# Kernel tuning notes

Hardware: AMD Instinct MI355X
Metric: run time of the kernel (lower is better)

The kernel has to match this reference:

```python
import jax, jax.numpy as jnp
import numpy as np

B_, T_, DIM = 32, 65536, 64
L_ = T_ // DIM                       # 1024 tokens after unfold
EXPAND, HEADDIM, DSTATE, DCONV = 4, 64, 16, 4
DIN = EXPAND * DIM                   # 256
NHEADS = DIN // HEADDIM              # 4
CONVDIM = DIN + 2 * DSTATE           # 288 (x, B, C share the conv)
DINPROJ = 2 * DIN + 2 * DSTATE + NHEADS  # 548
EPS = 1e-5


def setup_inputs() -> dict:
    key = jax.random.key(0)
    ks = jax.random.split(key, 8)
    x = jax.random.normal(ks[0], (B_, T_), jnp.float32)
    in_proj_w = jax.random.normal(ks[1], (DINPROJ, DIM), jnp.float32) * (DIM ** -0.5)
    conv_w = jax.random.normal(ks[2], (CONVDIM, DCONV), jnp.float32) * (DCONV ** -0.5)
    conv_b = jax.random.normal(ks[3], (CONVDIM,), jnp.float32) * 0.01
    # dt_bias so that softplus(dt_bias) ~ dt in [1e-3, 1e-1] (standard Mamba init)
    dt_bias = jnp.log(jnp.expm1(jax.random.uniform(ks[4], (NHEADS,), minval=0.001, maxval=0.1)))
    A_log = jnp.log(jax.random.uniform(ks[5], (NHEADS,), minval=1.0, maxval=16.0))
    D = jnp.ones((NHEADS,), jnp.float32)
    norm_gate_w = jnp.ones((DIN,), jnp.float32)
    out_proj_w = jax.random.normal(ks[6], (DIM, DIN), jnp.float32) * (DIN ** -0.5)
    block_norm_w = jnp.ones((DIM,), jnp.float32)
    return dict(x=x, in_proj_w=in_proj_w, conv_w=conv_w, conv_b=conv_b,
                dt_bias=dt_bias, A_log=A_log, D=D, norm_gate_w=norm_gate_w,
                out_proj_w=out_proj_w, block_norm_w=block_norm_w)


def _rmsnorm(x, w, eps=EPS):
    return x * jax.lax.rsqrt(jnp.mean(x * x, axis=-1, keepdims=True) + eps) * w


def _mamba2(u, in_proj_w, conv_w, conv_b, dt_bias, A_log, D, norm_gate_w, out_proj_w):
    # u: (b, l, d_model)
    b, l, _ = u.shape
    zxbcdt = jnp.einsum('bld,ed->ble', u, in_proj_w)            # (b,l,548)
    z, xBC, dt = jnp.split(zxbcdt, [DIN, DIN + CONVDIM], axis=-1)
    dt = jax.nn.softplus(dt + dt_bias)                           # (b,l,h)
    # causal depthwise conv1d (kernel DCONV) + SiLU
    xp = jnp.pad(xBC, ((0, 0), (DCONV - 1, 0), (0, 0)))
    xc = conv_b + sum(xp[:, k:k + l, :] * conv_w[:, k] for k in range(DCONV))
    xBC = jax.nn.silu(xc)
    xs, Bm, Cm = jnp.split(xBC, [DIN, DIN + DSTATE], axis=-1)    # (b,l,256),(b,l,16),(b,l,16)
    xh = xs.reshape(b, l, NHEADS, HEADDIM)                       # (b,l,h,p)
    A = -jnp.exp(A_log)                                          # (h,)

    def step(h, inp):
        x_t, dt_t, B_t, C_t = inp                                # (b,h,p),(b,h),(b,n),(b,n)
        dA = jnp.exp(dt_t * A)                                   # (b,h)
        h = h * dA[..., None, None] + dt_t[..., None, None] * x_t[..., None] * B_t[:, None, None, :]
        y = jnp.einsum('bhpn,bn->bhp', h, C_t)
        return h, y

    h0 = jnp.zeros((b, NHEADS, HEADDIM, DSTATE), u.dtype)
    _, ys = jax.lax.scan(step, h0, (xh.transpose(1, 0, 2, 3), dt.transpose(1, 0, 2),
                                    Bm.transpose(1, 0, 2), Cm.transpose(1, 0, 2)))
    y = ys.transpose(1, 0, 2, 3) + D[:, None] * xh               # (b,l,h,p) skip term
    y = y.reshape(b, l, DIN)
    y = _rmsnorm(y * jax.nn.silu(z), norm_gate_w)                # RMSNormGated
    return jnp.einsum('ble,de->bld', y, out_proj_w)              # (b,l,d_model)


def reference(x, in_proj_w, conv_w, conv_b, dt_bias, A_log, D, norm_gate_w,
              out_proj_w, block_norm_w):
    B, T = x.shape
    batch = x.reshape(B, L_, DIM)                                # unfold(1, dim, dim)
    # Block(fused_add_norm=False, n_layer=1): residual=batch; hidden=mixer(norm(batch))
    hidden = _mamba2(_rmsnorm(batch, block_norm_w), in_proj_w, conv_w, conv_b,
                     dt_bias, A_log, D, norm_gate_w, out_proj_w)
    residual = hidden + batch                                    # forward_f + for_residual
    out = residual.reshape(B, T) + x                             # flatten + input residual
    return out
```

## Files before the change

kernel.cpp:

```cpp
#include <hip/hip_runtime.h>
#include <math.h>

#define BB 32
#define LL 1024
#define DIMM 64
#define DINN 256
#define NHEADS 4
#define DSTATE 16
#define DINPROJ 548
#define EPSF 1e-5f
#define NCH 16
#define CS 64

typedef __attribute__((ext_vector_type(8))) short bf16x8;
typedef __attribute__((ext_vector_type(4))) float f32x4;

__device__ inline ushort f2bf(float f) {
    union { float f; unsigned u; } v; v.f = f;
    unsigned r = (v.u + 0x7FFFu + ((v.u >> 16) & 1u)) >> 16;
    return (ushort)r;
}
__device__ inline float bf2f(ushort u) {
    union { float f; unsigned u; } v; v.u = ((unsigned)u) << 16; return v.f;
}
__device__ inline float fexp(float v) { return __expf(v); }
__device__ inline float fsilu(float v) {
    return v * __builtin_amdgcn_rcpf(1.f + __expf(-v));
}

__global__ __launch_bounds__(256) void kwcvt(
        const float* __restrict__ Win, const float* __restrict__ Wout,
        ushort* __restrict__ Wb, ushort* __restrict__ Wob) {
    int i = blockIdx.x * 256 + threadIdx.x;
    if (i < DINPROJ * 64) Wb[i] = f2bf(Win[i]);
    else if (i < DINPROJ * 64 + 64 * DINN) {
        int j = i - DINPROJ * 64;
        Wob[j] = f2bf(Wout[j]);
    }
}

__global__ __launch_bounds__(256) void k1_mfma(
        const float* __restrict__ x, const ushort* __restrict__ Wb,
        const float* __restrict__ bnw, const float* __restrict__ Wfp,
        const float* __restrict__ dt_bias,
        ushort* __restrict__ xbcbuf, float* __restrict__ dtbuf) {
    __shared__ __align__(16) union {
        struct { float u[32][68]; float wdt[4][68]; } a;
        ushort ob[32][296];
    } s;
    __shared__ float rstd[32];
    const int t = threadIdx.x;
    const int m0 = blockIdx.x * 32;
    const int b = m0 >> 10;
    const int lbase = m0 & 1023;

    const float* xrow = x + (size_t)m0 * 64;
    #pragma unroll
    for (int i = 0; i < 2; ++i) {
        int idx = t + i * 256;
        float4 v = ((const float4*)xrow)[idx];
        *(float4*)&s.a.u[idx >> 4][(idx & 15) * 4] = v;
    }
    s.a.wdt[t >> 6][t & 63] = Wfp[(size_t)(544 + (t >> 6)) * 64 + (t & 63)] * bnw[t & 63];
    __syncthreads();
    {
        int row = t >> 3, part = t & 7;
        float ss = 0.f;
        #pragma unroll
        for (int j = 0; j < 8; ++j) { float v = s.a.u[row][part * 8 + j]; ss = fmaf(v, v, ss); }
        ss += __shfl_xor(ss, 1); ss += __shfl_xor(ss, 2); ss += __shfl_xor(ss, 4);
        if (part == 0) rstd[row] = rsqrtf(ss * (1.f / 64.f) + EPSF);
    }
    __syncthreads();

    const int w = t >> 6, l = t & 63;
    const int a = l & 15, kb = (l >> 4) * 8;

    float4 bw[2][2];
    bw[0][0] = *(const float4*)&bnw[kb];
    bw[0][1] = *(const float4*)&bnw[kb + 4];
    bw[1][0] = *(const float4*)&bnw[32 + kb];
    bw[1][1] = *(const float4*)&bnw[32 + kb + 4];

    bf16x8 af[2][2];
    #pragma unroll
    for (int mt = 0; mt < 2; ++mt) {
        float rs = rstd[mt * 16 + a];
        #pragma unroll
        for (int kk = 0; kk < 2; ++kk) {
            float4 v0 = *(const float4*)&s.a.u[mt * 16 + a][kk * 32 + kb];
            float4 v1 = *(const float4*)&s.a.u[mt * 16 + a][kk * 32 + kb + 4];
            ushort* p = (ushort*)&af[mt][kk];
            p[0] = f2bf(v0.x * rs * bw[kk][0].x);
            p[1] = f2bf(v0.y * rs * bw[kk][0].y);
            p[2] = f2bf(v0.z * rs * bw[kk][0].z);
            p[3] = f2bf(v0.w * rs * bw[kk][0].w);
            p[4] = f2bf(v1.x * rs * bw[kk][1].x);
            p[5] = f2bf(v1.y * rs * bw[kk][1].y);
            p[6] = f2bf(v1.z * rs * bw[kk][1].z);
            p[7] = f2bf(v1.w * rs * bw[kk][1].w);
        }
    }

    if (t < 128) {
        int row = t >> 2, h = t & 3;
        const float* ur = s.a.u[row];
        const float* wr = s.a.wdt[h];
        float sd = 0.f;
        #pragma unroll
        for (int k4 = 0; k4 < 16; ++k4) {
            float4 uv = *(const float4*)&ur[k4 * 4];
            float4 wv = *(const float4*)&wr[k4 * 4];
            sd = fmaf(uv.x, wv.x, sd); sd = fmaf(uv.y, wv.y, sd);
            sd = fmaf(uv.z, wv.z, sd); sd = fmaf(uv.w, wv.w, sd);
        }
        sd = sd * rstd[row] + dt_bias[h];
        sd = fmaxf(sd, 0.f) + log1pf(expf(-fabsf(sd)));
        dtbuf[((size_t)(b * 4 + h)) * LL + lbase + row] = sd;
    }
    __syncthreads();

    for (int nt = 16 + w; nt < 34; nt += 4) {
        const ushort* wbp = Wb + (size_t)(nt * 16 + a) * 64 + kb;
        bf16x8 b0 = *(const bf16x8*)wbp;
        bf16x8 b1 = *(const bf16x8*)(wbp + 32);
        #pragma unroll
        for (int mt = 0; mt < 2; ++mt) {
            f32x4 acc = {0.f, 0.f, 0.f, 0.f};
            acc = __builtin_amdgcn_mfma_f32_16x16x32_bf16(af[mt][0], b0, acc, 0, 0, 0);
            acc = __builtin_amdgcn_mfma_f32_16x16x32_bf16(af[mt][1], b1, acc, 0, 0, 0);
            int row0 = mt * 16 + (l >> 4) * 4;
            int col = nt * 16 + a - 256;
            #pragma unroll
            for (int r = 0; r < 4; ++r) s.ob[row0 + r][col] = f2bf(acc[r]);
        }
    }
    __syncthreads();

    for (int i = t; i < 1152; i += 256) {
        int row = i / 36, c8 = (i % 36) * 8;
        *(uint4*)&xbcbuf[(size_t)(m0 + row) * 288 + c8] = *(const uint4*)&s.ob[row][c8];
    }
}

__global__ __launch_bounds__(256) void k3a_ssd(
        const ushort* __restrict__ xbcbuf, const float* __restrict__ dtbuf,
        const float* __restrict__ conv_w, const float* __restrict__ conv_b,
        const float* __restrict__ A_log, const float* __restrict__ Dp,
        ushort* __restrict__ y, float* __restrict__ h0buf,
        float* __restrict__ cdecbuf, ushort* __restrict__ Cpost) {
    const int bid = blockIdx.x;
    const int c = bid & 15, h = (bid >> 4) & 3, b = bid >> 6;
    const int t = threadIdx.x;

    __shared__ __align__(16) union {
        struct { ushort rawx[67][64]; ushort rawbc[67][32]; } st;
        struct { ushort Mb[64][72]; ushort BwT[16][72]; } ssd;
    } uu;
    __shared__ ushort XbT[64][72];
    __shared__ ushort Bb[64][40];
    __shared__ ushort Cb[64][40];
    __shared__ float dtt[64], laa[64], ww[64];

    const float A  = -expf(A_log[h]);
    const float Dh = Dp[h];
    const int l0 = c * CS;
    const ushort* xb = xbcbuf + (size_t)b * LL * 288;

    for (int i = t; i < 67 * 32; i += 256) {
        int r = i >> 5, cu = i & 31;
        int l = l0 - 3 + r;
        ((uint*)&uu.st.rawx[r][0])[cu] =
            (l >= 0) ? ((const uint*)(xb + (size_t)l * 288 + h * 64))[cu] : 0u;
    }
    for (int i = t; i < 67 * 16; i += 256) {
        int r = i >> 4, cu = i & 15;
        int l = l0 - 3 + r;
        ((uint*)&uu.st.rawbc[r][0])[cu] =
            (l >= 0) ? ((const uint*)(xb + (size_t)l * 288 + 256))[cu] : 0u;
    }
    for (int i = t; i < 512; i += 256) {
        int r = i >> 3, cc = i & 7;
        ((uint*)&Bb[r][16])[cc] = 0;
        ((uint*)&Cb[r][16])[cc] = 0;
    }
    if (t < 64) {
        float dv = dtbuf[((size_t)(b * 4 + h)) * LL + l0 + t];
        float run = dv * A;
        #pragma unroll
        for (int off = 1; off < 64; off <<= 1) {
            float o = __shfl_up(run, off, 64);
            if (t >= off) run += o;
        }
        dtt[t] = dv;
        laa[t] = run;
        cdecbuf[((size_t)(b * 4 + h)) * LL + l0 + t] = fexp(run);
        float laEnd = __shfl(run, 63, 64);
        ww[t] = dv * fexp(laEnd - run);
    }
    __syncthreads();

    {
        const int jx = t & 63;
        const int w0 = (t >> 6) * 16;
        const int cx = h * 64 + jx;
        const float4 cwx = *(const float4*)&conv_w[cx * 4];
        const float  cbx = conv_b[cx];
        float r0[19];
        #pragma unroll
        for (int k = 0; k < 19; ++k) r0[k] = bf2f(uu.st.rawx[w0 + k][jx]);
        ushort vv[16];
        #pragma unroll
        for (int k = 0; k < 16; ++k) {
            float v = cbx + r0[k] * cwx.x + r0[k + 1] * cwx.y
                          + r0[k + 2] * cwx.z + r0[k + 3] * cwx.w;
            vv[k] = f2bf(fsilu(v));
        }
        *(bf16x8*)&XbT[jx][w0]     = *(bf16x8*)&vv[0];
        *(bf16x8*)&XbT[jx][w0 + 8] = *(bf16x8*)&vv[8];

        const int jbc = t & 31, cbc = 256 + jbc;
        const float4 cwb = *(const float4*)&conv_w[cbc * 4];
        const float  cbb = conv_b[cbc];
        #pragma unroll
        for (int i = 0; i < 8; ++i) {
            int ss = (t >> 5) + i * 8;
            float v = cbb + bf2f(uu.st.rawbc[ss][jbc]) * cwb.x
                          + bf2f(uu.st.rawbc[ss + 1][jbc]) * cwb.y
                          + bf2f(uu.st.rawbc[ss + 2][jbc]) * cwb.z
                          + bf2f(uu.st.rawbc[ss + 3][jbc]) * cwb.w;
            v = fsilu(v);
            if (jbc < 16) Bb[ss][jbc] = f2bf(v);
            else {
                ushort bv = f2bf(v);
                Cb[ss][jbc - 16] = bv;
                Cpost[((size_t)b * LL + l0 + ss) * DSTATE + (jbc - 16)] = bv;
            }
        }
    }
    __syncthreads();

    const int w = t >> 6, l = t & 63;
    const int fr = l & 15, fq = l >> 4;

    f32x4 gacc[4];
    {
        bf16x8 ca = *(const bf16x8*)&Cb[w * 16 + fr][fq * 8];
        #pragma unroll
        for (int jt = 0; jt < 4; ++jt) {
            bf16x8 bb = *(const bf16x8*)&Bb[jt * 16 + fr][fq * 8];
            f32x4 z = {0.f, 0.f, 0.f, 0.f};
            gacc[jt] = __builtin_amdgcn_mfma_f32_16x16x32_bf16(ca, bb, z, 0, 0, 0);
        }
    }
    #pragma unroll
    for (int jt = 0; jt < 4; ++jt) {
        int j = jt * 16 + fr;
        float laj = laa[j], dtj = dtt[j];
        #pragma unroll
        for (int r = 0; r < 4; ++r) {
            int i = w * 16 + fq * 4 + r;
            float m = (j <= i) ? gacc[jt][r] * fexp(laa[i] - laj) * dtj : 0.f;
            uu.ssd.Mb[i][j] = f2bf(m);
        }
    }
    #pragma unroll
    for (int i2 = 0; i2 < 4; ++i2) {
        int idx = t + i2 * 256;
        int n = idx & 15, jj = idx >> 4;
        uu.ssd.BwT[n][jj] = f2bf(ww[jj] * bf2f(Bb[jj][n]));
    }

    {
        bf16x8 ma0 = *(const bf16x8*)&uu.ssd.Mb[w * 16 + fr][fq * 8];
        bf16x8 ma1 = *(const bf16x8*)&uu.ssd.Mb[w * 16 + fr][32 + fq * 8];
        #pragma unroll
        for (int pt = 0; pt < 4; ++pt) {
            bf16x8 xb0 = *(const bf16x8*)&XbT[pt * 16 + fr][fq * 8];
            bf16x8 xb1 = *(const bf16x8*)&XbT[pt * 16 + fr][32 + fq * 8];
            f32x4 acc = {0.f, 0.f, 0.f, 0.f};
            acc = __builtin_amdgcn_mfma_f32_16x16x32_bf16(ma0, xb0, acc, 0, 0, 0);
            acc = __builtin_amdgcn_mfma_f32_16x16x32_bf16(ma1, xb1, acc, 0, 0, 0);
            #pragma unroll
            for (int r = 0; r < 4; ++r) {
                int i = w * 16 + fq * 4 + r;
                int p = pt * 16 + fr;
                float xv = bf2f(XbT[p][i]);
                uu.ssd.Mb[i][p] = f2bf(acc[r] + Dh * xv);
            }
        }
    }
    __syncthreads();

    if (c < 15) {
        bf16x8 xa0 = *(const bf16x8*)&XbT[w * 16 + fr][fq * 8];
        bf16x8 xa1 = *(const bf16x8*)&XbT[w * 16 + fr][32 + fq * 8];
        bf16x8 bw0 = *(const bf16x8*)&uu.ssd.BwT[fr][fq * 8];
        bf16x8 bw1 = *(const bf16x8*)&uu.ssd.BwT[fr][32 + fq * 8];
        f32x4 acc = {0.f, 0.f, 0.f, 0.f};
        acc = __builtin_amdgcn_mfma_f32_16x16x32_bf16(xa0, bw0, acc, 0, 0, 0);
        acc = __builtin_amdgcn_mfma_f32_16x16x32_bf16(xa1, bw1, acc, 0, 0, 0);
        float* Sdst = h0buf + (((size_t)(b * 4 + h)) * NCH + (c + 1)) * 1024;
        #pragma unroll
        for (int r = 0; r < 4; ++r) {
            int p = w * 16 + fq * 4 + r;
            Sdst[p * 16 + fr] = acc[r];
        }
    }

    {
        ushort* ybase = y + ((size_t)b * LL + l0) * DINN + h * 64;
        #pragma unroll
        for (int ii = 0; ii < 2; ++ii) {
            int idx = t + ii * 256;
            int row = idx >> 3, c8 = (idx & 7) * 8;
            *(uint4*)&ybase[(size_t)row * DINN + c8] = *(const uint4*)&uu.ssd.Mb[row][c8];
        }
    }
}

__global__ __launch_bounds__(256) void k3b_chunkscan(
        float* __restrict__ h0buf, const float* __restrict__ cdecbuf) {
    const int bh = blockIdx.x;
    const int t = threadIdx.x;
    float* base = h0buf + (size_t)bh * NCH * 1024;
    const float* cd = cdecbuf + (size_t)bh * LL;
    float4 run = {0.f, 0.f, 0.f, 0.f};
    *(float4*)&base[(size_t)t * 4] = run;
    #pragma unroll
    for (int c = 1; c < NCH; ++c) {
        float P = cd[c * CS - 1];
        float4 S = *(float4*)&base[(size_t)c * 1024 + t * 4];
        run.x = fmaf(run.x, P, S.x);
        run.y = fmaf(run.y, P, S.y);
        run.z = fmaf(run.z, P, S.z);
        run.w = fmaf(run.w, P, S.w);
        *(float4*)&base[(size_t)c * 1024 + t * 4] = run;
    }
}

__global__ __launch_bounds__(256) void k4_out(
        const ushort* __restrict__ ybf, const float* __restrict__ ngw,
        const ushort* __restrict__ Wob, const ushort* __restrict__ Wb,
        const float* __restrict__ bnw, const float* __restrict__ x,
        const float* __restrict__ h0buf, const float* __restrict__ cdecbuf,
        const ushort* __restrict__ Cpost, float* __restrict__ out) {
    __shared__ __align__(16) union {
        float u[64][68];
        ushort zg[64][264];
    } s;
    __shared__ float Cs[64][16];
    __shared__ float cds[64][4];
    __shared__ float rstd[64];
    const int t = threadIdx.x;
    const int m0 = blockIdx.x * 64;
    const int b  = m0 >> 10;
    const int l0 = m0 & 1023;
    const int ck = l0 >> 6;
    const ushort* yb = ybf + (size_t)m0 * DINN;

    const int ch4 = (t & 63) * 4;
    const int hh  = ch4 >> 6;
    const int p0  = ch4 & 63;
    const float* hbase = h0buf + (((size_t)(b * 4 + hh)) * NCH + ck) * 1024 + p0 * 16;
    float4 H[4][4];
    #pragma unroll
    for (int k = 0; k < 4; ++k)
        #pragma unroll
        for (int n4 = 0; n4 < 4; ++n4)
            H[k][n4] = *(const float4*)&hbase[k * 16 + n4 * 4];

    const float* xrow = x + (size_t)m0 * 64;
    #pragma unroll
    for (int i = 0; i < 4; ++i) {
        int idx = t + i * 256;
        float4 v = ((const float4*)xrow)[idx];
        *(float4*)&s.u[idx >> 4][(idx & 15) * 4] = v;
    }
    {
        int r = t >> 2, n0 = (t & 3) * 4;
        ushort4 cu4 = *(const ushort4*)&Cpost[((size_t)b * LL + l0 + r) * DSTATE + n0];
        Cs[r][n0 + 0] = bf2f(cu4.x);
        Cs[r][n0 + 1] = bf2f(cu4.y);
        Cs[r][n0 + 2] = bf2f(cu4.z);
        Cs[r][n0 + 3] = bf2f(cu4.w);
        int hh2 = t & 3;
        cds[r][hh2] = cdecbuf[((size_t)(b * 4 + hh2)) * LL + l0 + r];
    }
    __syncthreads();

    {
        int row = t >> 2, part = t & 3;
        float ss = 0.f;
        #pragma unroll
        for (int j = 0; j < 16; ++j) { float v = s.u[row][part * 16 + j]; ss = fmaf(v, v, ss); }
        ss += __shfl_xor(ss, 1); ss += __shfl_xor(ss, 2);
        if (part == 0) rstd[row] = rsqrtf(ss * (1.f / 64.f) + EPSF);
    }
    __syncthreads();

    const int w = t >> 6, l = t & 63;
    const int a = l & 15, kb = (l >> 4) * 8;
    float4 bw[2][2];
    bw[0][0] = *(const float4*)&bnw[kb];
    bw[0][1] = *(const float4*)&bnw[kb + 4];
    bw[1][0] = *(const float4*)&bnw[32 + kb];
    bw[1][1] = *(const float4*)&bnw[32 + kb + 4];
    bf16x8 af[4][2];
    #pragma unroll
    for (int mt = 0; mt < 4; ++mt) {
        float rs = rstd[mt * 16 + a];
        #pragma unroll
        for (int kk = 0; kk < 2; ++kk) {
            float4 v0 = *(const float4*)&s.u[mt * 16 + a][kk * 32 + kb];
            float4 v1 = *(const float4*)&s.u[mt * 16 + a][kk * 32 + kb + 4];
            ushort* p = (ushort*)&af[mt][kk];
            p[0] = f2bf(v0.x * rs * bw[kk][0].x);
            p[1] = f2bf(v0.y * rs * bw[kk][0].y);
            p[2] = f2bf(v0.z * rs * bw[kk][0].z);
            p[3] = f2bf(v0.w * rs * bw[kk][0].w);
            p[4] = f2bf(v1.x * rs * bw[kk][1].x);
            p[5] = f2bf(v1.y * rs * bw[kk][1].y);
            p[6] = f2bf(v1.z * rs * bw[kk][1].z);
            p[7] = f2bf(v1.w * rs * bw[kk][1].w);
        }
    }
    __syncthreads();

    #pragma unroll
    for (int ct4 = 0; ct4 < 4; ++ct4) {
        int ct = w * 4 + ct4;
        const ushort* wbp = Wb + (size_t)(ct * 16 + a) * 64 + kb;
        bf16x8 b0 = *(const bf16x8*)wbp;
        bf16x8 b1 = *(const bf16x8*)(wbp + 32);
        #pragma unroll
        for (int mt = 0; mt < 4; ++mt) {
            f32x4 acc = {0.f, 0.f, 0.f, 0.f};
            acc = __builtin_amdgcn_mfma_f32_16x16x32_bf16(af[mt][0], b0, acc, 0, 0, 0);
            acc = __builtin_amdgcn_mfma_f32_16x16x32_bf16(af[mt][1], b1, acc, 0, 0, 0);
            int row0 = mt * 16 + (l >> 4) * 4;
            int col = ct * 16 + a;
            #pragma unroll
            for (int r = 0; r < 4; ++r) s.zg[row0 + r][col] = f2bf(fsilu(acc[r]));
        }
    }
    __syncthreads();

    const float4 ng4 = *(const float4*)&ngw[ch4];

    #pragma unroll
    for (int i = 0; i < 16; ++i) {
        int row = i * 4 + (t >> 6);
        ushort4 yu = *(const ushort4*)&yb[(size_t)row * DINN + ch4];
        ushort4 zu = *(const ushort4*)&s.zg[row][ch4];
        float4 yv = { bf2f(yu.x), bf2f(yu.y), bf2f(yu.z), bf2f(yu.w) };
        float4 zv = { bf2f(zu.x), bf2f(zu.y), bf2f(zu.z), bf2f(zu.w) };
        float4 C0 = *(const float4*)&Cs[row][0];
        float4 C1 = *(const float4*)&Cs[row][4];
        float4 C2 = *(const float4*)&Cs[row][8];
        float4 C3 = *(const float4*)&Cs[row][12];
        float cdv = cds[row][hh];
        float corr[4];
        #pragma unroll
        for (int k = 0; k < 4; ++k) {
            float sc = H[k][0].x * C0.x + H[k][0].y * C0.y + H[k][0].z * C0.z + H[k][0].w * C0.w;
            sc += H[k][1].x * C1.x + H[k][1].y * C1.y + H[k][1].z * C1.z + H[k][1].w * C1.w;
            sc += H[k][2].x * C2.x + H[k][2].y * C2.y + H[k][2].z * C2.z + H[k][2].w * C2.w;
            sc += H[k][3].x * C3.x + H[k][3].y * C3.y + H[k][3].z * C3.z + H[k][3].w * C3.w;
            corr[k] = sc * cdv;
        }
        float4 gv;
        gv.x = (yv.x + corr[0]) * zv.x;
        gv.y = (yv.y + corr[1]) * zv.y;
        gv.z = (yv.z + corr[2]) * zv.z;
        gv.w = (yv.w + corr[3]) * zv.w;
        float sq = gv.x * gv.x + gv.y * gv.y + gv.z * gv.z + gv.w * gv.w;
        sq += __shfl_xor(sq, 1);  sq += __shfl_xor(sq, 2);  sq += __shfl_xor(sq, 4);
        sq += __shfl_xor(sq, 8);  sq += __shfl_xor(sq, 16); sq += __shfl_xor(sq, 32);
        float rs = rsqrtf(sq * (1.f / 256.f) + EPSF);
        ushort4 o;
        o.x = f2bf(gv.x * rs * ng4.x);
        o.y = f2bf(gv.y * rs * ng4.y);
        o.z = f2bf(gv.z * rs * ng4.z);
        o.w = f2bf(gv.w * rs * ng4.w);
        *(ushort4*)&s.zg[row][ch4] = o;
    }
    __syncthreads();

    const int j = l & 15;
    bf16x8 bf[8];
    #pragma unroll
    for (int ks = 0; ks < 8; ++ks)
        bf[ks] = *(const bf16x8*)&Wob[(size_t)(16 * w + j) * DINN + ks * 32 + kb];
    #pragma unroll
    for (int mt = 0; mt < 4; ++mt) {
        f32x4 acc = {0.f, 0.f, 0.f, 0.f};
        #pragma unroll
        for (int ks = 0; ks < 8; ++ks) {
            bf16x8 ag = *(const bf16x8*)&s.zg[mt * 16 + j][ks * 32 + kb];
            acc = __builtin_amdgcn_mfma_f32_16x16x32_bf16(ag, bf[ks], acc, 0, 0, 0);
        }
        #pragma unroll
        for (int r = 0; r < 4; ++r) {
            size_t row = (size_t)m0 + mt * 16 + (l >> 4) * 4 + r;
            size_t oidx = row * 64 + 16 * w + j;
            out[oidx] = acc[r] + 2.f * x[oidx];
        }
    }
}

extern "C" void kernel_launch(void* const* d_in, const int* in_sizes, int n_in,
                              void* d_out, int out_size, void* d_ws, size_t ws_size,
                              hipStream_t stream) {
    const float* x          = (const float*)d_in[0];
    const float* in_proj_w  = (const float*)d_in[1];
    const float* conv_w     = (const float*)d_in[2];
    const float* conv_b     = (const float*)d_in[3];
    const float* dt_bias    = (const float*)d_in[4];
    const float* A_log      = (const float*)d_in[5];
    const float* D          = (const float*)d_in[6];
    const float* norm_gate  = (const float*)d_in[7];
    const float* out_proj_w = (const float*)d_in[8];
    const float* block_norm = (const float*)d_in[9];
    float* out = (float*)d_out;

    float* h0b   = (float*)d_ws;
    float* cdec  = h0b  + (size_t)BB * NHEADS * NCH * 1024;
    float* dtb   = cdec + (size_t)BB * NHEADS * LL;
    ushort* Cp   = (ushort*)(dtb + (size_t)BB * NHEADS * LL);
    ushort* ybf  = Cp   + (size_t)BB * LL * DSTATE;
    ushort* xbc  = ybf  + (size_t)BB * LL * DINN;
    ushort* Wb   = xbc  + (size_t)BB * LL * 288;
    ushort* Wob  = Wb   + (size_t)DINPROJ * 64;

    kwcvt<<<201, 256, 0, stream>>>(in_proj_w, out_proj_w, Wb, Wob);
    k1_mfma<<<1024, 256, 0, stream>>>(x, Wb, block_norm, in_proj_w, dt_bias, xbc, dtb);
    k3a_ssd<<<2048, 256, 0, stream>>>(xbc, dtb, conv_w, conv_b, A_log, D, ybf, h0b, cdec, Cp);
    k3b_chunkscan<<<128, 256, 0, stream>>>(h0b, cdec);
    k4_out<<<512, 256, 0, stream>>>(ybf, norm_gate, Wob, Wb, block_norm, x, h0b, cdec, Cp, out);
}
```

Baseline: 68.98 us.

## Fuse weight conversion and chunk-state scan into consumer kernels, cutting launches

Removes the separate fp32-to-bf16 weight conversion kernel: k1 and k4 now load fp32 weights and pack them to bf16 in registers. Removes the inter-chunk scan kernel: each k4 block recomputes its incoming chunk state by serially accumulating the preceding chunk states, which makes the work uneven across chunks (up to 15 steps for the last chunk). k1 tiles grow from 32 to 64 rows with half the blocks, and k4 reuses x from shared memory for the residual instead of re-reading it from global memory. Together these aim to cut two kernel launches and their global round trips, paid for with redundant state reads and repeated weight conversion in every block.

```diff
diff --git a/kernel.cpp b/kernel.cpp
--- a/kernel.cpp
+++ b/kernel.cpp
@@ -27,36 +27,30 @@
 __device__ inline float fsilu(float v) {
     return v * __builtin_amdgcn_rcpf(1.f + __expf(-v));
 }
-
-__global__ __launch_bounds__(256) void kwcvt(
-        const float* __restrict__ Win, const float* __restrict__ Wout,
-        ushort* __restrict__ Wb, ushort* __restrict__ Wob) {
-    int i = blockIdx.x * 256 + threadIdx.x;
-    if (i < DINPROJ * 64) Wb[i] = f2bf(Win[i]);
-    else if (i < DINPROJ * 64 + 64 * DINN) {
-        int j = i - DINPROJ * 64;
-        Wob[j] = f2bf(Wout[j]);
-    }
+__device__ inline bf16x8 pack8(float4 a, float4 b) {
+    bf16x8 r; ushort* p = (ushort*)&r;
+    p[0] = f2bf(a.x); p[1] = f2bf(a.y); p[2] = f2bf(a.z); p[3] = f2bf(a.w);
+    p[4] = f2bf(b.x); p[5] = f2bf(b.y); p[6] = f2bf(b.z); p[7] = f2bf(b.w);
+    return r;
 }
 
 __global__ __launch_bounds__(256) void k1_mfma(
-        const float* __restrict__ x, const ushort* __restrict__ Wb,
-        const float* __restrict__ bnw, const float* __restrict__ Wfp,
-        const float* __restrict__ dt_bias,
+        const float* __restrict__ x, const float* __restrict__ Wfp,
+        const float* __restrict__ bnw, const float* __restrict__ dt_bias,
         ushort* __restrict__ xbcbuf, float* __restrict__ dtbuf) {
     __shared__ __align__(16) union {
-        struct { float u[32][68]; float wdt[4][68]; } a;
-        ushort ob[32][296];
+        struct { float u[64][68]; float wdt[4][68]; } a;
+        ushort ob[64][296];
     } s;
-    __shared__ float rstd[32];
+    __shared__ float rstd[64];
     const int t = threadIdx.x;
-    const int m0 = blockIdx.x * 32;
+    const int m0 = blockIdx.x * 64;
     const int b = m0 >> 10;
     const int lbase = m0 & 1023;
 
     const float* xrow = x + (size_t)m0 * 64;
     #pragma unroll
-    for (int i = 0; i < 2; ++i) {
+    for (int i = 0; i < 4; ++i) {
         int idx = t + i * 256;
         float4 v = ((const float4*)xrow)[idx];
         *(float4*)&s.a.u[idx >> 4][(idx & 15) * 4] = v;
@@ -64,11 +58,11 @@
     s.a.wdt[t >> 6][t & 63] = Wfp[(size_t)(544 + (t >> 6)) * 64 + (t & 63)] * bnw[t & 63];
     __syncthreads();
     {
-        int row = t >> 3, part = t & 7;
+        int row = t >> 2, part = t & 3;
         float ss = 0.f;
         #pragma unroll
-        for (int j = 0; j < 8; ++j) { float v = s.a.u[row][part * 8 + j]; ss = fmaf(v, v, ss); }
-        ss += __shfl_xor(ss, 1); ss += __shfl_xor(ss, 2); ss += __shfl_xor(ss, 4);
+        for (int j = 0; j < 16; ++j) { float v = s.a.u[row][part * 16 + j]; ss = fmaf(v, v, ss); }
+        ss += __shfl_xor(ss, 1); ss += __shfl_xor(ss, 2);
         if (part == 0) rstd[row] = rsqrtf(ss * (1.f / 64.f) + EPSF);
     }
     __syncthreads();
@@ -82,9 +76,9 @@
     bw[1][0] = *(const float4*)&bnw[32 + kb];
     bw[1][1] = *(const float4*)&bnw[32 + kb + 4];
 
-    bf16x8 af[2][2];
-    #pragma unroll
-    for (int mt = 0; mt < 2; ++mt) {
+    bf16x8 af[4][2];
+    #pragma unroll
+    for (int mt = 0; mt < 4; ++mt) {
         float rs = rstd[mt * 16 + a];
         #pragma unroll
         for (int kk = 0; kk < 2; ++kk) {
@@ -102,7 +96,7 @@
         }
     }
 
-    if (t < 128) {
+    {
         int row = t >> 2, h = t & 3;
         const float* ur = s.a.u[row];
         const float* wr = s.a.wdt[h];
@@ -121,11 +115,11 @@
     __syncthreads();
 
     for (int nt = 16 + w; nt < 34; nt += 4) {
-        const ushort* wbp = Wb + (size_t)(nt * 16 + a) * 64 + kb;
-        bf16x8 b0 = *(const bf16x8*)wbp;
-        bf16x8 b1 = *(const bf16x8*)(wbp + 32);
-        #pragma unroll
-        for (int mt = 0; mt < 2; ++mt) {
+        const float* wrow = Wfp + (size_t)(nt * 16 + a) * 64 + kb;
+        bf16x8 b0 = pack8(*(const float4*)&wrow[0],  *(const float4*)&wrow[4]);
+        bf16x8 b1 = pack8(*(const float4*)&wrow[32], *(const float4*)&wrow[36]);
+        #pragma unroll
+        for (int mt = 0; mt < 4; ++mt) {
             f32x4 acc = {0.f, 0.f, 0.f, 0.f};
             acc = __builtin_amdgcn_mfma_f32_16x16x32_bf16(af[mt][0], b0, acc, 0, 0, 0);
             acc = __builtin_amdgcn_mfma_f32_16x16x32_bf16(af[mt][1], b1, acc, 0, 0, 0);
@@ -137,7 +131,7 @@
     }
     __syncthreads();
 
-    for (int i = t; i < 1152; i += 256) {
+    for (int i = t; i < 2304; i += 256) {
         int row = i / 36, c8 = (i % 36) * 8;
         *(uint4*)&xbcbuf[(size_t)(m0 + row) * 288 + c8] = *(const uint4*)&s.ob[row][c8];
     }
@@ -319,29 +313,9 @@
     }
 }
 
-__global__ __launch_bounds__(256) void k3b_chunkscan(
-        float* __restrict__ h0buf, const float* __restrict__ cdecbuf) {
-    const int bh = blockIdx.x;
-    const int t = threadIdx.x;
-    float* base = h0buf + (size_t)bh * NCH * 1024;
-    const float* cd = cdecbuf + (size_t)bh * LL;
-    float4 run = {0.f, 0.f, 0.f, 0.f};
-    *(float4*)&base[(size_t)t * 4] = run;
-    #pragma unroll
-    for (int c = 1; c < NCH; ++c) {
-        float P = cd[c * CS - 1];
-        float4 S = *(float4*)&base[(size_t)c * 1024 + t * 4];
-        run.x = fmaf(run.x, P, S.x);
-        run.y = fmaf(run.y, P, S.y);
-        run.z = fmaf(run.z, P, S.z);
-        run.w = fmaf(run.w, P, S.w);
-        *(float4*)&base[(size_t)c * 1024 + t * 4] = run;
-    }
-}
-
 __global__ __launch_bounds__(256) void k4_out(
         const ushort* __restrict__ ybf, const float* __restrict__ ngw,
-        const ushort* __restrict__ Wob, const ushort* __restrict__ Wb,
+        const float* __restrict__ Wofp, const float* __restrict__ Wfp,
         const float* __restrict__ bnw, const float* __restrict__ x,
         const float* __restrict__ h0buf, const float* __restrict__ cdecbuf,
         const ushort* __restrict__ Cpost, float* __restrict__ out) {
@@ -359,16 +333,12 @@
     const int ck = l0 >> 6;
     const ushort* yb = ybf + (size_t)m0 * DINN;
 
-    const int ch4 = (t & 63) * 4;
+    const int w = t >> 6, l = t & 63;
+    const int ch4 = l * 4;
     const int hh  = ch4 >> 6;
     const int p0  = ch4 & 63;
-    const float* hbase = h0buf + (((size_t)(b * 4 + hh)) * NCH + ck) * 1024 + p0 * 16;
-    float4 H[4][4];
-    #pragma unroll
-    for (int k = 0; k < 4; ++k)
-        #pragma unroll
-        for (int n4 = 0; n4 < 4; ++n4)
-            H[k][n4] = *(const float4*)&hbase[k * 16 + n4 * 4];
+    const int a = l & 15, kb = (l >> 4) * 8;
+    const int j = l & 15;
 
     const float* xrow = x + (size_t)m0 * 64;
     #pragma unroll
@@ -387,20 +357,40 @@
         int hh2 = t & 3;
         cds[r][hh2] = cdecbuf[((size_t)(b * 4 + hh2)) * LL + l0 + r];
     }
+
+    float4 H[4][4];
+    #pragma unroll
+    for (int k = 0; k < 4; ++k)
+        #pragma unroll
+        for (int n4 = 0; n4 < 4; ++n4)
+            H[k][n4] = make_float4(0.f, 0.f, 0.f, 0.f);
+    for (int cc = 1; cc <= ck; ++cc) {
+        float P = cdecbuf[((size_t)(b * 4 + hh)) * LL + cc * CS - 1];
+        const float* sb = h0buf + (((size_t)(b * 4 + hh)) * NCH + cc) * 1024 + p0 * 16;
+        #pragma unroll
+        for (int k = 0; k < 4; ++k) {
+            #pragma unroll
+            for (int n4 = 0; n4 < 4; ++n4) {
+                float4 S = *(const float4*)&sb[k * 16 + n4 * 4];
+                H[k][n4].x = fmaf(H[k][n4].x, P, S.x);
+                H[k][n4].y = fmaf(H[k][n4].y, P, S.y);
+                H[k][n4].z = fmaf(H[k][n4].z, P, S.z);
+                H[k][n4].w = fmaf(H[k][n4].w, P, S.w);
+            }
+        }
+    }
     __syncthreads();
 
     {
         int row = t >> 2, part = t & 3;
         float ss = 0.f;
         #pragma unroll
-        for (int j = 0; j < 16; ++j) { float v = s.u[row][part * 16 + j]; ss = fmaf(v, v, ss); }
+        for (int jj = 0; jj < 16; ++jj) { float v = s.u[row][part * 16 + jj]; ss = fmaf(v, v, ss); }
         ss += __shfl_xor(ss, 1); ss += __shfl_xor(ss, 2);
         if (part == 0) rstd[row] = rsqrtf(ss * (1.f / 64.f) + EPSF);
     }
     __syncthreads();
 
-    const int w = t >> 6, l = t & 63;
-    const int a = l & 15, kb = (l >> 4) * 8;
     float4 bw[2][2];
     bw[0][0] = *(const float4*)&bnw[kb];
     bw[0][1] = *(const float4*)&bnw[kb + 4];
@@ -425,14 +415,20 @@
             p[7] = f2bf(v1.w * rs * bw[kk][1].w);
         }
     }
+    float xres[16];
+    #pragma unroll
+    for (int mt = 0; mt < 4; ++mt)
+        #pragma unroll
+        for (int r = 0; r < 4; ++r)
+            xres[mt * 4 + r] = s.u[mt * 16 + (l >> 4) * 4 + r][16 * w + j];
     __syncthreads();
 
     #pragma unroll
     for (int ct4 = 0; ct4 < 4; ++ct4) {
         int ct = w * 4 + ct4;
-        const ushort* wbp = Wb + (size_t)(ct * 16 + a) * 64 + kb;
-        bf16x8 b0 = *(const bf16x8*)wbp;
-        bf16x8 b1 = *(const bf16x8*)(wbp + 32);
+        const float* wrow = Wfp + (size_t)(ct * 16 + a) * 64 + kb;
+        bf16x8 b0 = pack8(*(const float4*)&wrow[0],  *(const float4*)&wrow[4]);
+        bf16x8 b1 = pack8(*(const float4*)&wrow[32], *(const float4*)&wrow[36]);
         #pragma unroll
         for (int mt = 0; mt < 4; ++mt) {
             f32x4 acc = {0.f, 0.f, 0.f, 0.f};
@@ -450,7 +446,7 @@
 
     #pragma unroll
     for (int i = 0; i < 16; ++i) {
-        int row = i * 4 + (t >> 6);
+        int row = i * 4 + w;
         ushort4 yu = *(const ushort4*)&yb[(size_t)row * DINN + ch4];
         ushort4 zu = *(const ushort4*)&s.zg[row][ch4];
         float4 yv = { bf2f(yu.x), bf2f(yu.y), bf2f(yu.z), bf2f(yu.w) };
@@ -487,11 +483,12 @@
     }
     __syncthreads();
 
-    const int j = l & 15;
     bf16x8 bf[8];
     #pragma unroll
-    for (int ks = 0; ks < 8; ++ks)
-        bf[ks] = *(const bf16x8*)&Wob[(size_t)(16 * w + j) * DINN + ks * 32 + kb];
+    for (int ks = 0; ks < 8; ++ks) {
+        const float* wo = Wofp + (size_t)(16 * w + j) * DINN + ks * 32 + kb;
+        bf[ks] = pack8(*(const float4*)&wo[0], *(const float4*)&wo[4]);
+    }
     #pragma unroll
     for (int mt = 0; mt < 4; ++mt) {
         f32x4 acc = {0.f, 0.f, 0.f, 0.f};
@@ -504,7 +501,7 @@
         for (int r = 0; r < 4; ++r) {
             size_t row = (size_t)m0 + mt * 16 + (l >> 4) * 4 + r;
             size_t oidx = row * 64 + 16 * w + j;
-            out[oidx] = acc[r] + 2.f * x[oidx];
+            out[oidx] = acc[r] + 2.f * xres[mt * 4 + r];
         }
     }
 }
@@ -530,12 +527,8 @@
     ushort* Cp   = (ushort*)(dtb + (size_t)BB * NHEADS * LL);
     ushort* ybf  = Cp   + (size_t)BB * LL * DSTATE;
     ushort* xbc  = ybf  + (size_t)BB * LL * DINN;
-    ushort* Wb   = xbc  + (size_t)BB * LL * 288;
-    ushort* Wob  = Wb   + (size_t)DINPROJ * 64;
-
-    kwcvt<<<201, 256, 0, stream>>>(in_proj_w, out_proj_w, Wb, Wob);
-    k1_mfma<<<1024, 256, 0, stream>>>(x, Wb, block_norm, in_proj_w, dt_bias, xbc, dtb);
+
+    k1_mfma<<<512, 256, 0, stream>>>(x, in_proj_w, block_norm, dt_bias, xbc, dtb);
     k3a_ssd<<<2048, 256, 0, stream>>>(xbc, dtb, conv_w, conv_b, A_log, D, ybf, h0b, cdec, Cp);
-    k3b_chunkscan<<<128, 256, 0, stream>>>(h0b, cdec);
-    k4_out<<<512, 256, 0, stream>>>(ybf, norm_gate, Wob, Wb, block_norm, x, h0b, cdec, Cp, out);
-}
+    k4_out<<<512, 256, 0, stream>>>(ybf, norm_gate, out_proj_w, in_proj_w, block_norm, x, h0b, cdec, Cp, out);
+}
```

After: 118.3 us. 71.4% more time.
